# Performance work log

Hardware: AMD Instinct MI355X
Metric: run time of the kernel (lower is better)

Reference implementation:

```python
import jax, jax.numpy as jnp
import numpy as np

E_DIM = 64
N_EMBED = 1024
N_TOKENS = 262144


def setup_inputs() -> dict:
    key = jax.random.key(0)
    k1, k2 = jax.random.split(key)
    inp = jax.random.normal(k1, (N_TOKENS, E_DIM), dtype=jnp.float32)
    # codebook init mirrors torch uniform_(-1/n_embed, 1/n_embed)
    embed = jax.random.uniform(k2, (E_DIM, N_EMBED), dtype=jnp.float32,
                               minval=-1.0 / N_EMBED, maxval=1.0 / N_EMBED)
    return {"input": inp, "embed": embed}


def reference(input, embed):
    e_dim, n_embed = embed.shape
    flatten = input.reshape(-1, e_dim)  # [N, e_dim]
    dist = (jnp.sum(flatten * flatten, axis=1, keepdims=True)
            - 2.0 * flatten @ embed
            + jnp.sum(embed * embed, axis=0, keepdims=True))
    embed_idxs = jnp.argmin(dist, axis=1)  # matches (-dist).max(1) indices
    embed_idxs = embed_idxs.reshape(input.shape[:-1])
    quantize = jnp.take(embed.T, embed_idxs, axis=0)  # gather codes -> [..., e_dim]
    # straight-through estimator
    quantize_input_grad = input + jax.lax.stop_gradient(quantize - input)
    return (quantize, input, quantize_input_grad, embed_idxs, embed)
```

## Files before the change

kernel.cpp:

```cpp
#include <hip/hip_runtime.h>
#include <hip/hip_bf16.h>
#include <math.h>

#define E_DIM    64
#define N_EMBED  1024
#define N_TOKENS 262144
#define FQCAP    32768

typedef __attribute__((ext_vector_type(8)))  short bf16x8;
typedef __attribute__((ext_vector_type(16))) float f32x16;


__device__ __forceinline__ short f2bf_bits(float f) {
    __hip_bfloat16 h = __float2bfloat16(f);
    return *reinterpret_cast<short*>(&h);
}
__device__ __forceinline__ float bfbits2f(short s) {
    unsigned int u = ((unsigned int)(unsigned short)s) << 16;
    return __uint_as_float(u);
}

__device__ __forceinline__ float exact_d(const float* __restrict__ xrow,
                                         const float* __restrict__ emb,
                                         const float* __restrict__ csum,
                                         float a, int j) {
#pragma clang fp contract(off)
    float b = 0.f;
#pragma unroll
    for (int k = 0; k < E_DIM; ++k) b = fmaf(xrow[k], emb[k * N_EMBED + j], b);
    return (a - 2.0f * b) + csum[j];
}

__device__ __forceinline__ float a_np_of(const float* x) {
#pragma clang fp contract(off)
    float s[16];
#pragma unroll
    for (int i = 0; i < 16; ++i)
        s[i] = (x[i] * x[i] + x[i + 16] * x[i + 16]) +
               (x[i + 32] * x[i + 32] + x[i + 48] * x[i + 48]);
    float hh[8];
#pragma unroll
    for (int i = 0; i < 8; ++i) hh[i] = s[i] + s[i + 8];
    float uu[4];
#pragma unroll
    for (int i = 0; i < 4; ++i) uu[i] = hh[i] + hh[i + 4];
    return (uu[0] + uu[2]) + (uu[1] + uu[3]);
}

__device__ __forceinline__ bool lexless(float av, int ai, float bv, int bi) {
    return (av < bv) || (av == bv && ai < bi);
}

__global__ __launch_bounds__(256) void vq_prep(const float* __restrict__ emb,
                                               short* __restrict__ eTc,
                                               float* __restrict__ out_e,
                                               float* __restrict__ c_out) {
    const int b = blockIdx.x;
    if (b < 256) {
        const int t = b * 256 + threadIdx.x;
        const int k = t >> 10, n = t & 1023;
        float e = emb[t];
        float m2 = -2.0f * e;
        short hb = f2bf_bits(m2);
        short lb = f2bf_bits(m2 - bfbits2f(hb));
        const int chunk = n >> 7, code = n & 127, slot = k >> 3, jj = k & 7;
        const int base = chunk * 16384 + (slot * 128 + code) * 8 + jj;
        eTc[base]        = hb;
        eTc[base + 8192] = lb;
        out_e[t] = e;
    } else {
#pragma clang fp contract(off)
        const int j = (b - 256) * 256 + threadIdx.x;
        float e = emb[j];
        float s = e * e;
        for (int k = 1; k < E_DIM; ++k) {
            float ek = emb[k * N_EMBED + j];
            float pk = ek * ek;
            s = s + pk;
        }
        c_out[j] = s;
    }
}

__device__ __forceinline__ void tile_epilogue(
    const f32x16& acc, const float* __restrict__ cvp16, int codebase_global,
    int h, float& v1, float& v2, float& v3, int& i1, int& i2) {
#pragma unroll
    for (int r = 0; r < 16; ++r) {
        const int row = (r & 3) + 8 * (r >> 2) + 4 * h;
        const float d = acc[r] + cvp16[r];
        const int idx = codebase_global + row;
        if (d < v3) {
            if (d < v1)      { v3 = v2; v2 = v1; i2 = i1; v1 = d; i1 = idx; }
            else if (d < v2) { v3 = v2; v2 = d;  i2 = idx; }
            else             { v3 = d; }
        }
    }
}

__global__ __launch_bounds__(256, 4) void vq_screen_kernel(
    const float* __restrict__ in, const float* __restrict__ emb,
    const float* __restrict__ csum, const short* __restrict__ eTc,
    float* __restrict__ out_idx,
    unsigned int* __restrict__ qcnt, unsigned int* __restrict__ fullQ)
{
    __shared__ uint4 lds_e[2048];

    const int t = threadIdx.x;
    const int wave = t >> 6, l = t & 63, col = l & 31, h = l >> 5;
    const int tok = blockIdx.x * 128 + wave * 32 + col;
    const float* xrow = in + (size_t)tok * E_DIM;

    float xv[4][8];
#pragma unroll
    for (int s = 0; s < 4; ++s) {
        float4 u0 = *reinterpret_cast<const float4*>(xrow + s * 16 + h * 8);
        float4 u1 = *reinterpret_cast<const float4*>(xrow + s * 16 + h * 8 + 4);
        xv[s][0] = u0.x; xv[s][1] = u0.y; xv[s][2] = u0.z; xv[s][3] = u0.w;
        xv[s][4] = u1.x; xv[s][5] = u1.y; xv[s][6] = u1.z; xv[s][7] = u1.w;
    }
    bf16x8 bhi[4], blo[4];
    float sax_h = 0.f;
#pragma unroll
    for (int s = 0; s < 4; ++s) {
#pragma unroll
        for (int j = 0; j < 8; ++j) {
            float x = xv[s][j];
            sax_h += fabsf(x);
            short hb = f2bf_bits(x);
            bhi[s][j] = hb;
            blo[s][j] = f2bf_bits(x - bfbits2f(hb));
        }
    }
    const float sax = sax_h + __shfl_xor(sax_h, 32, 64);

    float a_np;
    {
#pragma clang fp contract(off)
        float sv[8];
#pragma unroll
        for (int j = 0; j < 8; ++j) {
            float p0 = xv[0][j] * xv[0][j];
            float p1 = xv[1][j] * xv[1][j];
            float p2 = xv[2][j] * xv[2][j];
            float p3 = xv[3][j] * xv[3][j];
            sv[j] = (p0 + p1) + (p2 + p3);
        }
        float hh[8];
#pragma unroll
        for (int j = 0; j < 8; ++j) hh[j] = sv[j] + __shfl_xor(sv[j], 32, 64);
        float u0 = hh[0] + hh[4], u1 = hh[1] + hh[5];
        float u2 = hh[2] + hh[6], u3 = hh[3] + hh[7];
        a_np = (u0 + u2) + (u1 + u3);
    }

    float v1 = 3.4e38f, v2 = 3.4e38f, v3 = 3.4e38f;
    int i1 = 0, i2 = 0;

    for (int cc = 0; cc < 8; ++cc) {
        __syncthreads();
        {
            const uint4* gsrc = reinterpret_cast<const uint4*>(eTc) + cc * 2048;
#pragma unroll
            for (int j = 0; j < 8; ++j) lds_e[j * 256 + t] = gsrc[j * 256 + t];
        }
        __syncthreads();

        const int cb = cc << 7;
#pragma unroll
        for (int tp = 0; tp < 2; ++tp) {
            const int c0 = tp * 64 + col;
            f32x16 accA, accB;
#pragma unroll
            for (int r = 0; r < 16; ++r) { accA[r] = 0.f; accB[r] = 0.f; }
#pragma unroll
            for (int s = 0; s < 4; ++s) {
                const int slot = 2 * s + h;
                bf16x8 ahA = *reinterpret_cast<const bf16x8*>(&lds_e[slot * 128 + c0]);
                bf16x8 alA = *reinterpret_cast<const bf16x8*>(&lds_e[1024 + slot * 128 + c0]);
                bf16x8 ahB = *reinterpret_cast<const bf16x8*>(&lds_e[slot * 128 + c0 + 32]);
                bf16x8 alB = *reinterpret_cast<const bf16x8*>(&lds_e[1024 + slot * 128 + c0 + 32]);
                accA = __builtin_amdgcn_mfma_f32_32x32x16_bf16(ahA, bhi[s], accA, 0, 0, 0);
                accB = __builtin_amdgcn_mfma_f32_32x32x16_bf16(ahB, bhi[s], accB, 0, 0, 0);
                accA = __builtin_amdgcn_mfma_f32_32x32x16_bf16(ahA, blo[s], accA, 0, 0, 0);
                accB = __builtin_amdgcn_mfma_f32_32x32x16_bf16(ahB, blo[s], accB, 0, 0, 0);
                accA = __builtin_amdgcn_mfma_f32_32x32x16_bf16(alA, bhi[s], accA, 0, 0, 0);
                accB = __builtin_amdgcn_mfma_f32_32x32x16_bf16(alB, bhi[s], accB, 0, 0, 0);
            }
            float cvpA[16], cvpB[16];
#pragma unroll
            for (int g = 0; g < 4; ++g) {
                const float4 ca = *reinterpret_cast<const float4*>(&csum[cb + tp * 64 + 8 * g + 4 * h]);
                const float4 cbv4 = *reinterpret_cast<const float4*>(&csum[cb + tp * 64 + 32 + 8 * g + 4 * h]);
                cvpA[g*4+0] = ca.x;   cvpA[g*4+1] = ca.y;   cvpA[g*4+2] = ca.z;   cvpA[g*4+3] = ca.w;
                cvpB[g*4+0] = cbv4.x; cvpB[g*4+1] = cbv4.y; cvpB[g*4+2] = cbv4.z; cvpB[g*4+3] = cbv4.w;
            }
            tile_epilogue(accA, cvpA, cb + tp * 64,      h, v1, v2, v3, i1, i2);
            tile_epilogue(accB, cvpB, cb + tp * 64 + 32, h, v1, v2, v3, i1, i2);
        }
    }

    const float w1 = __shfl_xor(v1, 32, 64), w2 = __shfl_xor(v2, 32, 64), w3 = __shfl_xor(v3, 32, 64);
    const int   j1 = __shfl_xor(i1, 32, 64), j2 = __shfl_xor(i2, 32, 64);
    const bool bfirst = lexless(w1, j1, v1, i1);
    const float r1v = bfirst ? w1 : v1;  const int r1i = bfirst ? j1 : i1;
    const float cav = bfirst ? v1 : v2;  const int cai = bfirst ? i1 : i2;
    const float cbv = bfirst ? w2 : w1;  const int cbi = bfirst ? j2 : j1;
    const bool bsec = lexless(cbv, cbi, cav, cai);
    const float r2v = bsec ? cbv : cav;  const int r2i = bsec ? cbi : cai;
    const float r3v = bsec ? fminf(cav, bfirst ? w3 : w2)
                           : fminf(cbv, bfirst ? v2 : v3);

    if (l < 32) {
        const float thr = 8e-5f + 4e-7f * sax;
        const bool sane = (a_np < 150.f) && (sax < 128.f) && (fabsf(r1v) < 0.5f);
        int fin = r1i;
        if (sane && (r2v - r1v > thr)) {
        } else if (sane && (r3v - r1v > thr)) {
            const float d1 = exact_d(xrow, emb, csum, a_np, r1i);
            const float d2 = exact_d(xrow, emb, csum, a_np, r2i);
            if (d2 < d1 || (d2 == d1 && r2i < r1i)) fin = r2i;
        } else {
            const unsigned int qi = atomicAdd(qcnt, 1u);
            if (qi < FQCAP) fullQ[qi] = (unsigned int)tok;
        }
        out_idx[tok] = (float)fin;
    }
}

__global__ __launch_bounds__(256) void vq_full_kernel(
    const float* __restrict__ in, const float* __restrict__ emb,
    const float* __restrict__ csum, const unsigned int* __restrict__ qcnt,
    const unsigned int* __restrict__ fullQ, float* __restrict__ out_idx) {
#pragma clang fp contract(off)
    unsigned int nq = *qcnt;
    if (nq > FQCAP) nq = FQCAP;
    const int l = threadIdx.x & 63;
    for (unsigned int w = blockIdx.x * 4 + (threadIdx.x >> 6); w < nq; w += 1024) {
        const int tok = (int)fullQ[w];
        const float* xrow = in + (size_t)tok * E_DIM;
        float x[E_DIM];
#pragma unroll
        for (int j4 = 0; j4 < 16; ++j4) {
            const float4 u = *reinterpret_cast<const float4*>(xrow + j4 * 4);
            x[j4 * 4 + 0] = u.x; x[j4 * 4 + 1] = u.y;
            x[j4 * 4 + 2] = u.z; x[j4 * 4 + 3] = u.w;
        }
        const float a = a_np_of(x);
        const int c0 = l * 16;
        float b[16];
#pragma unroll
        for (int q = 0; q < 16; ++q) b[q] = 0.f;
        for (int k = 0; k < E_DIM; ++k) {
            const float xk = x[k];
            const float* er = emb + k * N_EMBED + c0;
#pragma unroll
            for (int q = 0; q < 16; ++q) b[q] = fmaf(xk, er[q], b[q]);
        }
        float bd = 3.4e38f; int bi = 1 << 30;
#pragma unroll
        for (int q = 0; q < 16; ++q) {
            const float d = (a - 2.0f * b[q]) + csum[c0 + q];
            if (d < bd) { bd = d; bi = c0 + q; }
        }
        for (int m = 1; m < 64; m <<= 1) {
            const float od = __shfl_xor(bd, m, 64);
            const int oi = __shfl_xor(bi, m, 64);
            if (od < bd || (od == bd && oi < bi)) { bd = od; bi = oi; }
        }
        if (l == 0) out_idx[tok] = (float)bi;
    }
}

__global__ __launch_bounds__(256) void vq_gather_kernel(
    const float* __restrict__ in, const float* __restrict__ emb,
    const float* __restrict__ idxf,
    float* __restrict__ out_q, float* __restrict__ out_in, float* __restrict__ out_g) {
#pragma clang fp contract(off)
    const size_t j = (size_t)blockIdx.x * 256 + threadIdx.x;
    const int m  = (int)(j >> 4);
    const int k0 = ((int)j & 15) * 4;
    const int idx = (int)idxf[m];

    const float4 x = reinterpret_cast<const float4*>(in)[j];
    const float q0 = emb[(size_t)(k0 + 0) * N_EMBED + idx];
    const float q1 = emb[(size_t)(k0 + 1) * N_EMBED + idx];
    const float q2 = emb[(size_t)(k0 + 2) * N_EMBED + idx];
    const float q3 = emb[(size_t)(k0 + 3) * N_EMBED + idx];

    float4 q = make_float4(q0, q1, q2, q3);
    float4 g;
    g.x = x.x + (q0 - x.x);
    g.y = x.y + (q1 - x.y);
    g.z = x.z + (q2 - x.z);
    g.w = x.w + (q3 - x.w);

    reinterpret_cast<float4*>(out_q)[j]  = q;
    reinterpret_cast<float4*>(out_in)[j] = x;
    reinterpret_cast<float4*>(out_g)[j]  = g;
}

extern "C" void kernel_launch(void* const* d_in, const int* in_sizes, int n_in,
                              void* d_out, int out_size, void* d_ws, size_t ws_size,
                              hipStream_t stream) {
    const float* in  = (const float*)d_in[0];
    const float* emb = (const float*)d_in[1];

    float* out     = (float*)d_out;
    float* out_q   = out;
    float* out_in  = out + (size_t)N_TOKENS * E_DIM;
    float* out_g   = out + 2ull * N_TOKENS * E_DIM;
    float* out_idx = out + 3ull * N_TOKENS * E_DIM;
    float* out_e   = out_idx + N_TOKENS;

    unsigned char* ws = (unsigned char*)d_ws;
    float*          c_ws  = (float*)(ws);
    short*          eTc   = (short*)(ws + 4096);
    unsigned int*   qcnt  = (unsigned int*)(ws + 4096 + 262144);
    unsigned int*   fullQ = (unsigned int*)(ws + 4096 + 262144 + 256);

    hipMemsetAsync(qcnt, 0, sizeof(unsigned int), stream);

    vq_prep<<<260, 256, 0, stream>>>(emb, eTc, out_e, c_ws);

    vq_screen_kernel<<<N_TOKENS / 128, 256, 0, stream>>>(
        in, emb, c_ws, eTc, out_idx, qcnt, fullQ);

    vq_full_kernel<<<256, 256, 0, stream>>>(in, emb, c_ws, qcnt, fullQ, out_idx);

    const int gather_blocks = (N_TOKENS * E_DIM / 4) / 256;
    vq_gather_kernel<<<gather_blocks, 256, 0, stream>>>(in, emb, out_idx,
                                                        out_q, out_in, out_g);
}
```

Measured before the change: 308.5 us.

## Drop codebook low-bf16 split, seed MFMA accumulators with norms, transpose codebook for gather

The screening GEMM now uses only the high bf16 part of the codebook, which cuts MFMA count from 6 to 4 per step and halves LDS staging. The code norms are loaded directly into the accumulators instead of being added in the epilogue. The screen threshold is widened to absorb the larger approximation error, which may send more tokens to the exact-check or full-search paths. A transposed fp32 codebook is written in prep so the gather kernel can read each code with one float4 load instead of four strided scalar loads.

```diff
diff --git a/kernel.cpp b/kernel.cpp
--- a/kernel.cpp
+++ b/kernel.cpp
@@ -54,6 +54,7 @@
 __global__ __launch_bounds__(256) void vq_prep(const float* __restrict__ emb,
                                                short* __restrict__ eTc,
                                                float* __restrict__ out_e,
+                                               float* __restrict__ embT,
                                                float* __restrict__ c_out) {
     const int b = blockIdx.x;
     if (b < 256) {
@@ -62,12 +63,10 @@
         float e = emb[t];
         float m2 = -2.0f * e;
         short hb = f2bf_bits(m2);
-        short lb = f2bf_bits(m2 - bfbits2f(hb));
         const int chunk = n >> 7, code = n & 127, slot = k >> 3, jj = k & 7;
-        const int base = chunk * 16384 + (slot * 128 + code) * 8 + jj;
-        eTc[base]        = hb;
-        eTc[base + 8192] = lb;
+        eTc[chunk * 8192 + (slot * 128 + code) * 8 + jj] = hb;
         out_e[t] = e;
+        embT[n * E_DIM + k] = e;
     } else {
 #pragma clang fp contract(off)
         const int j = (b - 256) * 256 + threadIdx.x;
@@ -83,12 +82,12 @@
 }
 
 __device__ __forceinline__ void tile_epilogue(
-    const f32x16& acc, const float* __restrict__ cvp16, int codebase_global,
-    int h, float& v1, float& v2, float& v3, int& i1, int& i2) {
+    const f32x16& acc, int codebase_global, int h,
+    float& v1, float& v2, float& v3, int& i1, int& i2) {
 #pragma unroll
     for (int r = 0; r < 16; ++r) {
         const int row = (r & 3) + 8 * (r >> 2) + 4 * h;
-        const float d = acc[r] + cvp16[r];
+        const float d = acc[r];
         const int idx = codebase_global + row;
         if (d < v3) {
             if (d < v1)      { v3 = v2; v2 = v1; i2 = i1; v1 = d; i1 = idx; }
@@ -104,7 +103,7 @@
     float* __restrict__ out_idx,
     unsigned int* __restrict__ qcnt, unsigned int* __restrict__ fullQ)
 {
-    __shared__ uint4 lds_e[2048];
+    __shared__ uint4 lds_e[1024];
 
     const int t = threadIdx.x;
     const int wave = t >> 6, l = t & 63, col = l & 31, h = l >> 5;
@@ -160,9 +159,9 @@
     for (int cc = 0; cc < 8; ++cc) {
         __syncthreads();
         {
-            const uint4* gsrc = reinterpret_cast<const uint4*>(eTc) + cc * 2048;
-#pragma unroll
-            for (int j = 0; j < 8; ++j) lds_e[j * 256 + t] = gsrc[j * 256 + t];
+            const uint4* gsrc = reinterpret_cast<const uint4*>(eTc) + cc * 1024;
+#pragma unroll
+            for (int j = 0; j < 4; ++j) lds_e[j * 256 + t] = gsrc[j * 256 + t];
         }
         __syncthreads();
 
@@ -170,33 +169,36 @@
 #pragma unroll
         for (int tp = 0; tp < 2; ++tp) {
             const int c0 = tp * 64 + col;
+            const int cbase = cb + tp * 64 + 4 * h;
+            const float4 cA0 = *reinterpret_cast<const float4*>(&csum[cbase + 0]);
+            const float4 cA1 = *reinterpret_cast<const float4*>(&csum[cbase + 8]);
+            const float4 cA2 = *reinterpret_cast<const float4*>(&csum[cbase + 16]);
+            const float4 cA3 = *reinterpret_cast<const float4*>(&csum[cbase + 24]);
+            const float4 cB0 = *reinterpret_cast<const float4*>(&csum[cbase + 32]);
+            const float4 cB1 = *reinterpret_cast<const float4*>(&csum[cbase + 40]);
+            const float4 cB2 = *reinterpret_cast<const float4*>(&csum[cbase + 48]);
+            const float4 cB3 = *reinterpret_cast<const float4*>(&csum[cbase + 56]);
             f32x16 accA, accB;
-#pragma unroll
-            for (int r = 0; r < 16; ++r) { accA[r] = 0.f; accB[r] = 0.f; }
+            accA[0]=cA0.x;  accA[1]=cA0.y;  accA[2]=cA0.z;  accA[3]=cA0.w;
+            accA[4]=cA1.x;  accA[5]=cA1.y;  accA[6]=cA1.z;  accA[7]=cA1.w;
+            accA[8]=cA2.x;  accA[9]=cA2.y;  accA[10]=cA2.z; accA[11]=cA2.w;
+            accA[12]=cA3.x; accA[13]=cA3.y; accA[14]=cA3.z; accA[15]=cA3.w;
+            accB[0]=cB0.x;  accB[1]=cB0.y;  accB[2]=cB0.z;  accB[3]=cB0.w;
+            accB[4]=cB1.x;  accB[5]=cB1.y;  accB[6]=cB1.z;  accB[7]=cB1.w;
+            accB[8]=cB2.x;  accB[9]=cB2.y;  accB[10]=cB2.z; accB[11]=cB2.w;
+            accB[12]=cB3.x; accB[13]=cB3.y; accB[14]=cB3.z; accB[15]=cB3.w;
 #pragma unroll
             for (int s = 0; s < 4; ++s) {
                 const int slot = 2 * s + h;
                 bf16x8 ahA = *reinterpret_cast<const bf16x8*>(&lds_e[slot * 128 + c0]);
-                bf16x8 alA = *reinterpret_cast<const bf16x8*>(&lds_e[1024 + slot * 128 + c0]);
                 bf16x8 ahB = *reinterpret_cast<const bf16x8*>(&lds_e[slot * 128 + c0 + 32]);
-                bf16x8 alB = *reinterpret_cast<const bf16x8*>(&lds_e[1024 + slot * 128 + c0 + 32]);
                 accA = __builtin_amdgcn_mfma_f32_32x32x16_bf16(ahA, bhi[s], accA, 0, 0, 0);
                 accB = __builtin_amdgcn_mfma_f32_32x32x16_bf16(ahB, bhi[s], accB, 0, 0, 0);
                 accA = __builtin_amdgcn_mfma_f32_32x32x16_bf16(ahA, blo[s], accA, 0, 0, 0);
                 accB = __builtin_amdgcn_mfma_f32_32x32x16_bf16(ahB, blo[s], accB, 0, 0, 0);
-                accA = __builtin_amdgcn_mfma_f32_32x32x16_bf16(alA, bhi[s], accA, 0, 0, 0);
-                accB = __builtin_amdgcn_mfma_f32_32x32x16_bf16(alB, bhi[s], accB, 0, 0, 0);
             }
-            float cvpA[16], cvpB[16];
-#pragma unroll
-            for (int g = 0; g < 4; ++g) {
-                const float4 ca = *reinterpret_cast<const float4*>(&csum[cb + tp * 64 + 8 * g + 4 * h]);
-                const float4 cbv4 = *reinterpret_cast<const float4*>(&csum[cb + tp * 64 + 32 + 8 * g + 4 * h]);
-                cvpA[g*4+0] = ca.x;   cvpA[g*4+1] = ca.y;   cvpA[g*4+2] = ca.z;   cvpA[g*4+3] = ca.w;
-                cvpB[g*4+0] = cbv4.x; cvpB[g*4+1] = cbv4.y; cvpB[g*4+2] = cbv4.z; cvpB[g*4+3] = cbv4.w;
-            }
-            tile_epilogue(accA, cvpA, cb + tp * 64,      h, v1, v2, v3, i1, i2);
-            tile_epilogue(accB, cvpB, cb + tp * 64 + 32, h, v1, v2, v3, i1, i2);
+            tile_epilogue(accA, cb + tp * 64,      h, v1, v2, v3, i1, i2);
+            tile_epilogue(accB, cb + tp * 64 + 32, h, v1, v2, v3, i1, i2);
         }
     }
 
@@ -212,7 +214,7 @@
                            : fminf(cbv, bfirst ? v2 : v3);
 
     if (l < 32) {
-        const float thr = 8e-5f + 4e-7f * sax;
+        const float thr = 8e-5f + 1.2e-5f * sax;
         const bool sane = (a_np < 150.f) && (sax < 128.f) && (fabsf(r1v) < 0.5f);
         int fin = r1i;
         if (sane && (r2v - r1v > thr)) {
@@ -273,7 +275,7 @@
 }
 
 __global__ __launch_bounds__(256) void vq_gather_kernel(
-    const float* __restrict__ in, const float* __restrict__ emb,
+    const float* __restrict__ in, const float* __restrict__ embT,
     const float* __restrict__ idxf,
     float* __restrict__ out_q, float* __restrict__ out_in, float* __restrict__ out_g) {
 #pragma clang fp contract(off)
@@ -283,17 +285,13 @@
     const int idx = (int)idxf[m];
 
     const float4 x = reinterpret_cast<const float4*>(in)[j];
-    const float q0 = emb[(size_t)(k0 + 0) * N_EMBED + idx];
-    const float q1 = emb[(size_t)(k0 + 1) * N_EMBED + idx];
-    const float q2 = emb[(size_t)(k0 + 2) * N_EMBED + idx];
-    const float q3 = emb[(size_t)(k0 + 3) * N_EMBED + idx];
-
-    float4 q = make_float4(q0, q1, q2, q3);
+    const float4 q = *reinterpret_cast<const float4*>(&embT[(size_t)idx * E_DIM + k0]);
+
     float4 g;
-    g.x = x.x + (q0 - x.x);
-    g.y = x.y + (q1 - x.y);
-    g.z = x.z + (q2 - x.z);
-    g.w = x.w + (q3 - x.w);
+    g.x = x.x + (q.x - x.x);
+    g.y = x.y + (q.y - x.y);
+    g.z = x.z + (q.z - x.z);
+    g.w = x.w + (q.w - x.w);
 
     reinterpret_cast<float4*>(out_q)[j]  = q;
     reinterpret_cast<float4*>(out_in)[j] = x;
@@ -316,12 +314,13 @@
     unsigned char* ws = (unsigned char*)d_ws;
     float*          c_ws  = (float*)(ws);
     short*          eTc   = (short*)(ws + 4096);
-    unsigned int*   qcnt  = (unsigned int*)(ws + 4096 + 262144);
-    unsigned int*   fullQ = (unsigned int*)(ws + 4096 + 262144 + 256);
+    float*          embT  = (float*)(ws + 4096 + 131072);
+    unsigned int*   qcnt  = (unsigned int*)(ws + 4096 + 131072 + 262144);
+    unsigned int*   fullQ = (unsigned int*)(ws + 4096 + 131072 + 262144 + 256);
 
     hipMemsetAsync(qcnt, 0, sizeof(unsigned int), stream);
 
-    vq_prep<<<260, 256, 0, stream>>>(emb, eTc, out_e, c_ws);
+    vq_prep<<<260, 256, 0, stream>>>(emb, eTc, out_e, embT, c_ws);
 
     vq_screen_kernel<<<N_TOKENS / 128, 256, 0, stream>>>(
         in, emb, c_ws, eTc, out_idx, qcnt, fullQ);
@@ -329,6 +328,6 @@
     vq_full_kernel<<<256, 256, 0, stream>>>(in, emb, c_ws, qcnt, fullQ, out_idx);
 
     const int gather_blocks = (N_TOKENS * E_DIM / 4) / 256;
-    vq_gather_kernel<<<gather_blocks, 256, 0, stream>>>(in, emb, out_idx,
+    vq_gather_kernel<<<gather_blocks, 256, 0, stream>>>(in, embT, out_idx,
                                                         out_q, out_in, out_g);
 }
```

New measurement: 942.8 us. 3.06x slower.
